# Optimization experiments

Measured on AMD Instinct MI355X. Metric: run time of the kernel, lower is better.

The kernel has to match this reference:

```python
import jax, jax.numpy as jnp
import numpy as np

N_OUT = 4096
N_IN = 4096
N_SPARSE = 1024  # int(0.25 * N_IN)
BATCH, SEQ = 4, 2048


def setup_inputs() -> dict:
    key = jax.random.key(0)
    k1, k2, k3 = jax.random.split(key, 3)
    x = jax.random.normal(k1, (BATCH, SEQ, N_IN), dtype=jnp.float32)
    sparse_values = jax.random.normal(k2, (N_OUT, N_SPARSE), dtype=jnp.float32)
    # static equivalent of the boolean sparse_mask: sorted unique column indices
    sparse_idx = jnp.sort(jax.random.permutation(k3, N_IN)[:N_SPARSE]).astype(jnp.int64)
    return {"x": x, "sparse_values": sparse_values, "sparse_idx": sparse_idx}


def reference(x, sparse_values, sparse_idx):
    # x[..., mask] @ sparse_values.T  ->  gather columns then GEMM
    x_g = jnp.take(x, sparse_idx, axis=-1)          # [B, S, n_sparse]
    return jnp.einsum('bsk,ok->bso', x_g, sparse_values)  # [B, S, n_out]
```

## Files before the change

### kernel.cpp

```cpp
#include <hip/hip_runtime.h>
#include <hip/hip_bf16.h>

#define NOUT  4096
#define KDIM  1024
#define MROWS 8192

typedef __attribute__((ext_vector_type(8))) short bf16x8;
typedef __attribute__((ext_vector_type(16))) float f32x16;

__device__ __forceinline__ unsigned short f2bf(float f) {
  union { float f; unsigned int u; } c; c.f = f;
  unsigned int lsb = (c.u >> 16) & 1u;
  c.u += 0x7fffu + lsb;
  return (unsigned short)(c.u >> 16);
}

__device__ __forceinline__ void gload_lds16(const void* g, void* l) {
  __builtin_amdgcn_global_load_lds(
      (const __attribute__((address_space(1))) void*)g,
      (__attribute__((address_space(3))) void*)l, 16, 0, 0);
}

#define FENCE() asm volatile("" ::: "memory")
#define BAR() do { FENCE(); __builtin_amdgcn_s_barrier(); FENCE(); } while (0)
#define VMW(n) asm volatile("s_waitcnt vmcnt(" #n ")" ::: "memory")

__global__ __launch_bounds__(512) void prep(const float* __restrict__ x,
                                            const void* __restrict__ idx_raw,
                                            const float* __restrict__ w,
                                            unsigned short* __restrict__ xg,
                                            unsigned short* __restrict__ wb) {
  const int b = blockIdx.x;
  const int t = threadIdx.x;

  if (b < 2048) {
    const long long* p64 = (const long long*)idx_raw;
    const bool is64 = ((unsigned long long)p64[0]) < 4096ull;
    const float* xb = x + (size_t)b * 4 * 4096;
    ushort4* dst = (ushort4*)(xg + (size_t)b * 4 * 1024);
#pragma unroll
    for (int i = 0; i < 2; ++i) {
      const int q = t + 512 * i;
      const int row = q >> 8;
      const int k = (q & 255) * 4;
      int ka0, ka1, ka2, ka3;
      if (is64) {
        longlong2 v0 = ((const longlong2*)p64)[(k >> 1) + 0];
        longlong2 v1 = ((const longlong2*)p64)[(k >> 1) + 1];
        ka0 = (int)v0.x; ka1 = (int)v0.y; ka2 = (int)v1.x; ka3 = (int)v1.y;
      } else {
        int4 v = ((const int4*)idx_raw)[k >> 2];
        ka0 = v.x; ka1 = v.y; ka2 = v.z; ka3 = v.w;
      }
      const float* rp = xb + row * 4096;
      ushort4 o;
      o.x = f2bf(rp[ka0]); o.y = f2bf(rp[ka1]);
      o.z = f2bf(rp[ka2]); o.w = f2bf(rp[ka3]);
      dst[q] = o;
    }
  } else {
    const int i0 = (b - 2048) * 2048 + t;
#pragma unroll
    for (int j = 0; j < 4; ++j) {
      float4 v = ((const float4*)w)[i0 + 512 * j];
      ushort4 o;
      o.x = f2bf(v.x); o.y = f2bf(v.y); o.z = f2bf(v.z); o.w = f2bf(v.w);
      ((ushort4*)wb)[i0 + 512 * j] = o;
    }
  }
}

__global__ __launch_bounds__(512, 2) void gemm256(const unsigned short* __restrict__ A,
                                                  const unsigned short* __restrict__ B,
                                                  float* __restrict__ C) {
  __shared__ __align__(16) unsigned short lds[65536];

  const int tid = threadIdx.x;
  const int lane = tid & 63;
  const int wid = tid >> 6;
  const int wm = wid >> 2, wn = wid & 3;
  const int l31 = lane & 31, lh = lane >> 5;

  const int bn0 = blockIdx.x * 256;
  const int bm0 = blockIdx.y * 256;

  const int pr = tid >> 3;
  const int cg = (tid & 7) ^ (pr & 7) ^ ((pr >> 3) & 3);
  const unsigned short* Ag = A + (size_t)(bm0 + pr) * KDIM + cg * 8;
  const unsigned short* Bg = B + (size_t)(bn0 + pr) * KDIM + cg * 8;
  const int tid8 = tid * 8;

  const int sw8 = (l31 & 7) ^ (l31 >> 3);
  const int cK0 = (lh ^ sw8) * 8;
  const int cK1 = cK0 ^ 16;
  const int cK2 = cK0 ^ 32;
  const int cK3 = cK0 ^ 48;
  const int aRow = wm * 8192 + l31 * 64;
  const int bRow = 32768 + wn * 4096 + l31 * 64;

  f32x16 acc[4][2] = {};
  bf16x8 a[2][4], bN0[4], bN1[4];

#define LOAD_A(D, MH) do {                                                        \
    const unsigned short* _p = lds + (D) * 16384 + aRow + (MH) * 4096;            \
    a[0][0] = *(const bf16x8*)(_p + cK0);        a[0][1] = *(const bf16x8*)(_p + cK1);         \
    a[0][2] = *(const bf16x8*)(_p + cK2);        a[0][3] = *(const bf16x8*)(_p + cK3);         \
    a[1][0] = *(const bf16x8*)(_p + 2048 + cK0); a[1][1] = *(const bf16x8*)(_p + 2048 + cK1);  \
    a[1][2] = *(const bf16x8*)(_p + 2048 + cK2); a[1][3] = *(const bf16x8*)(_p + 2048 + cK3);  \
  } while (0)

#define LOAD_B(D, NF, R) do {                                                     \
    const unsigned short* _p = lds + (D) * 16384 + bRow + (NF) * 2048;            \
    R[0] = *(const bf16x8*)(_p + cK0); R[1] = *(const bf16x8*)(_p + cK1);         \
    R[2] = *(const bf16x8*)(_p + cK2); R[3] = *(const bf16x8*)(_p + cK3);         \
  } while (0)

#define STAGE_A(D, T, H) do {                                                     \
    gload_lds16(Ag + (size_t)((H) * 128) * KDIM + (T) * 64,                       \
                lds + (D) * 16384 + (H) * 8192 + tid8);                           \
    gload_lds16(Ag + (size_t)((H) * 128 + 64) * KDIM + (T) * 64,                  \
                lds + (D) * 16384 + (H) * 8192 + 4096 + tid8);                    \
  } while (0)

#define STAGE_B(D, T, H) do {                                                     \
    gload_lds16(Bg + (size_t)((H) * 128) * KDIM + (T) * 64,                       \
                lds + 32768 + (D) * 16384 + (H) * 8192 + tid8);                   \
    gload_lds16(Bg + (size_t)((H) * 128 + 64) * KDIM + (T) * 64,                  \
                lds + 32768 + (D) * 16384 + (H) * 8192 + 4096 + tid8);            \
  } while (0)

#define MFMA_Q(MH, NH, R) do {                                                    \
    __builtin_amdgcn_s_setprio(1);                                                \
    _Pragma("unroll") for (int kb = 0; kb < 4; ++kb) {                            \
      _Pragma("unroll") for (int mf = 0; mf < 2; ++mf) {                          \
        acc[(MH)*2+mf][NH] = __builtin_amdgcn_mfma_f32_32x32x16_bf16(             \
            a[mf][kb], R[kb], acc[(MH)*2+mf][NH], 0, 0, 0);                       \
      }                                                                           \
    }                                                                             \
    __builtin_amdgcn_s_setprio(0);                                                \
  } while (0)

  STAGE_B(0, 0, 0); STAGE_B(0, 0, 1);
  STAGE_A(0, 0, 0); STAGE_A(0, 0, 1);
  STAGE_B(1, 1, 0); STAGE_B(1, 1, 1);
  VMW(4);
  BAR();

  for (int i = 0; i < 8; ++i) {
    const int tA1 = 2 * i + 1;
    const int tN0 = (2 * i + 2) & 15;
    const int tN1 = (2 * i + 3) & 15;

    LOAD_A(0, 0); LOAD_B(0, 0, bN0); STAGE_A(1, tA1, 0);
    BAR(); MFMA_Q(0, 0, bN0); BAR();
    LOAD_B(0, 1, bN1); STAGE_A(1, tA1, 1);
    BAR(); MFMA_Q(0, 1, bN1); BAR();
    LOAD_A(0, 1); STAGE_B(0, tN0, 0);
    BAR(); MFMA_Q(1, 0, bN0); BAR();
    STAGE_B(0, tN0, 1);
    BAR(); MFMA_Q(1, 1, bN1); VMW(4); BAR();
    LOAD_A(1, 0); LOAD_B(1, 0, bN0); STAGE_A(0, tN0, 0);
    BAR(); MFMA_Q(0, 0, bN0); BAR();
    LOAD_B(1, 1, bN1); STAGE_A(0, tN0, 1);
    BAR(); MFMA_Q(0, 1, bN1); BAR();
    LOAD_A(1, 1); STAGE_B(1, tN1, 0);
    BAR(); MFMA_Q(1, 0, bN0); BAR();
    STAGE_B(1, tN1, 1);
    BAR(); MFMA_Q(1, 1, bN1); VMW(4); BAR();
  }

  VMW(0);
  float* base = C + (size_t)(bm0 + wm * 128) * NOUT + bn0 + wn * 64;
#pragma unroll
  for (int mf = 0; mf < 4; ++mf)
#pragma unroll
    for (int nf = 0; nf < 2; ++nf) {
      f32x16 v = acc[mf][nf];
#pragma unroll
      for (int r = 0; r < 16; ++r) {
        const int rowi = mf * 32 + (r & 3) + 8 * (r >> 2) + 4 * lh;
        base[(size_t)rowi * NOUT + nf * 32 + l31] = v[r];
      }
    }

#undef LOAD_A
#undef LOAD_B
#undef STAGE_A
#undef STAGE_B
#undef MFMA_Q
}

extern "C" void kernel_launch(void* const* d_in, const int* in_sizes, int n_in,
                              void* d_out, int out_size, void* d_ws, size_t ws_size,
                              hipStream_t stream) {
  const float* x   = (const float*)d_in[0];
  const float* sv  = (const float*)d_in[1];
  const void*  idx = d_in[2];
  float* out = (float*)d_out;

  unsigned short* xg = (unsigned short*)d_ws;
  unsigned short* wb = xg + (size_t)MROWS * KDIM;

  prep<<<2560, 512, 0, stream>>>(x, idx, sv, xg, wb);

  dim3 grid(NOUT / 256, MROWS / 256);
  gemm256<<<grid, 512, 0, stream>>>(xg, wb, out);
}
```

Measured before the change: 114.6 us.

## Fuse column gather and bf16 conversion of x into the GEMM A-tile staging

Removes the separate gather/convert pass over x. The GEMM now loads the indexed fp32 columns directly from global memory into registers, converts them with packed bf16 conversion, and writes them to LDS, software-pipelined one stage ahead. Indices are cached in LDS, and the block-to-tile mapping is remapped so neighbouring blocks share x rows. This saves the intermediate write/read of the gathered activations, but each GEMM block reads x via scattered 4-byte loads that are re-fetched by every N-tile (16 blocks per M tile). It also raises register pressure and vmcnt bookkeeping.

```diff
diff --git a/kernel.cpp b/kernel.cpp
--- a/kernel.cpp
+++ b/kernel.cpp
@@ -15,6 +15,12 @@
   return (unsigned short)(c.u >> 16);
 }
 
+__device__ __forceinline__ unsigned cvtpk(float lo, float hi) {
+  unsigned r;
+  asm("v_cvt_pk_bf16_f32 %0, %1, %2" : "=v"(r) : "v"(lo), "v"(hi));
+  return r;
+}
+
 __device__ __forceinline__ void gload_lds16(const void* g, void* l) {
   __builtin_amdgcn_global_load_lds(
       (const __attribute__((address_space(1))) void*)g,
@@ -24,56 +30,27 @@
 #define FENCE() asm volatile("" ::: "memory")
 #define BAR() do { FENCE(); __builtin_amdgcn_s_barrier(); FENCE(); } while (0)
 #define VMW(n) asm volatile("s_waitcnt vmcnt(" #n ")" ::: "memory")
-
-__global__ __launch_bounds__(512) void prep(const float* __restrict__ x,
-                                            const void* __restrict__ idx_raw,
-                                            const float* __restrict__ w,
-                                            unsigned short* __restrict__ xg,
-                                            unsigned short* __restrict__ wb) {
-  const int b = blockIdx.x;
-  const int t = threadIdx.x;
-
-  if (b < 2048) {
-    const long long* p64 = (const long long*)idx_raw;
-    const bool is64 = ((unsigned long long)p64[0]) < 4096ull;
-    const float* xb = x + (size_t)b * 4 * 4096;
-    ushort4* dst = (ushort4*)(xg + (size_t)b * 4 * 1024);
-#pragma unroll
-    for (int i = 0; i < 2; ++i) {
-      const int q = t + 512 * i;
-      const int row = q >> 8;
-      const int k = (q & 255) * 4;
-      int ka0, ka1, ka2, ka3;
-      if (is64) {
-        longlong2 v0 = ((const longlong2*)p64)[(k >> 1) + 0];
-        longlong2 v1 = ((const longlong2*)p64)[(k >> 1) + 1];
-        ka0 = (int)v0.x; ka1 = (int)v0.y; ka2 = (int)v1.x; ka3 = (int)v1.y;
-      } else {
-        int4 v = ((const int4*)idx_raw)[k >> 2];
-        ka0 = v.x; ka1 = v.y; ka2 = v.z; ka3 = v.w;
-      }
-      const float* rp = xb + row * 4096;
-      ushort4 o;
-      o.x = f2bf(rp[ka0]); o.y = f2bf(rp[ka1]);
-      o.z = f2bf(rp[ka2]); o.w = f2bf(rp[ka3]);
-      dst[q] = o;
-    }
-  } else {
-    const int i0 = (b - 2048) * 2048 + t;
-#pragma unroll
-    for (int j = 0; j < 4; ++j) {
-      float4 v = ((const float4*)w)[i0 + 512 * j];
-      ushort4 o;
-      o.x = f2bf(v.x); o.y = f2bf(v.y); o.z = f2bf(v.z); o.w = f2bf(v.w);
-      ((ushort4*)wb)[i0 + 512 * j] = o;
-    }
+#define LGKM0() asm volatile("s_waitcnt lgkmcnt(0)" ::: "memory")
+
+__global__ __launch_bounds__(512) void prep_w(const float* __restrict__ w,
+                                              unsigned short* __restrict__ wb) {
+  const int i0 = blockIdx.x * 1024 + threadIdx.x;
+#pragma unroll
+  for (int j = 0; j < 2; ++j) {
+    const int i = i0 + 512 * j;
+    float4 v = ((const float4*)w)[i];
+    ushort4 o;
+    o.x = f2bf(v.x); o.y = f2bf(v.y); o.z = f2bf(v.z); o.w = f2bf(v.w);
+    ((ushort4*)wb)[i] = o;
   }
 }
 
-__global__ __launch_bounds__(512, 2) void gemm256(const unsigned short* __restrict__ A,
-                                                  const unsigned short* __restrict__ B,
-                                                  float* __restrict__ C) {
-  __shared__ __align__(16) unsigned short lds[65536];
+__global__ __launch_bounds__(512, 2) void gemmf(const float* __restrict__ x,
+                                                const void* __restrict__ idx_raw,
+                                                const unsigned short* __restrict__ Bw,
+                                                float* __restrict__ C) {
+  __shared__ __align__(16) unsigned short lds[65536 + 2048];
+  int* sidxB = (int*)(lds + 65536);
 
   const int tid = threadIdx.x;
   const int lane = tid & 63;
@@ -81,14 +58,29 @@
   const int wm = wid >> 2, wn = wid & 3;
   const int l31 = lane & 31, lh = lane >> 5;
 
-  const int bn0 = blockIdx.x * 256;
-  const int bm0 = blockIdx.y * 256;
+  const int bid = blockIdx.x;
+  const int bm0 = ((bid & 7) * 4 + (bid >> 7)) * 256;
+  const int bn0 = ((bid >> 3) & 15) * 256;
 
   const int pr = tid >> 3;
   const int cg = (tid & 7) ^ (pr & 7) ^ ((pr >> 3) & 3);
-  const unsigned short* Ag = A + (size_t)(bm0 + pr) * KDIM + cg * 8;
-  const unsigned short* Bg = B + (size_t)(bn0 + pr) * KDIM + cg * 8;
+  const unsigned short* Bg = Bw + (size_t)(bn0 + pr) * KDIM + cg * 8;
   const int tid8 = tid * 8;
+  const char* xb = (const char*)(x + (size_t)bm0 * 4096);
+
+  {
+    const long long* p64 = (const long long*)idx_raw;
+    const int* p32 = (const int*)idx_raw;
+    const bool is64 = ((unsigned long long)p64[0]) < 4096ull;
+    if (is64) {
+      sidxB[tid] = ((int)p64[tid]) << 2;
+      sidxB[tid + 512] = ((int)p64[tid + 512]) << 2;
+    } else {
+      sidxB[tid] = p32[tid] << 2;
+      sidxB[tid + 512] = p32[tid + 512] << 2;
+    }
+  }
+  LGKM0(); BAR();
 
   const int sw8 = (l31 & 7) ^ (l31 >> 3);
   const int cK0 = (lh ^ sw8) * 8;
@@ -100,6 +92,42 @@
 
   f32x16 acc[4][2] = {};
   bf16x8 a[2][4], bN0[4], bN1[4];
+  float gE0[16], gE1[16], gO0[16], gO1[16];
+
+#define LDX(boff) (*(const float*)(xb + (boff)))
+
+#define GA_ISSUE(T, H, S) do {                                                    \
+    const int _kb = (T) * 64 + cg * 8;                                            \
+    const int4 _o1 = *(const int4*)&sidxB[_kb];                                   \
+    const int4 _o2 = *(const int4*)&sidxB[_kb + 4];                               \
+    const int _r1 = ((H) * 128 + pr) << 14;                                       \
+    const int _r2 = _r1 + (64 << 14);                                             \
+    S[0] = LDX(_r1 + _o1.x);  S[1] = LDX(_r1 + _o1.y);                            \
+    S[2] = LDX(_r1 + _o1.z);  S[3] = LDX(_r1 + _o1.w);                            \
+    S[4] = LDX(_r1 + _o2.x);  S[5] = LDX(_r1 + _o2.y);                            \
+    S[6] = LDX(_r1 + _o2.z);  S[7] = LDX(_r1 + _o2.w);                            \
+    S[8] = LDX(_r2 + _o1.x);  S[9] = LDX(_r2 + _o1.y);                            \
+    S[10] = LDX(_r2 + _o1.z); S[11] = LDX(_r2 + _o1.w);                           \
+    S[12] = LDX(_r2 + _o2.x); S[13] = LDX(_r2 + _o2.y);                           \
+    S[14] = LDX(_r2 + _o2.z); S[15] = LDX(_r2 + _o2.w);                           \
+  } while (0)
+
+#define GA_WRITE(D, H, S) do {                                                    \
+    uint4 _u1, _u2;                                                               \
+    _u1.x = cvtpk(S[0], S[1]);   _u1.y = cvtpk(S[2], S[3]);                       \
+    _u1.z = cvtpk(S[4], S[5]);   _u1.w = cvtpk(S[6], S[7]);                       \
+    _u2.x = cvtpk(S[8], S[9]);   _u2.y = cvtpk(S[10], S[11]);                     \
+    _u2.z = cvtpk(S[12], S[13]); _u2.w = cvtpk(S[14], S[15]);                     \
+    *(uint4*)(lds + (D) * 16384 + (H) * 8192 + tid8) = _u1;                       \
+    *(uint4*)(lds + (D) * 16384 + (H) * 8192 + 4096 + tid8) = _u2;                \
+  } while (0)
+
+#define STAGE_B(D, T, H) do {                                                     \
+    gload_lds16(Bg + (size_t)((H) * 128) * KDIM + (T) * 64,                       \
+                lds + 32768 + (D) * 16384 + (H) * 8192 + tid8);                   \
+    gload_lds16(Bg + (size_t)((H) * 128 + 64) * KDIM + (T) * 64,                  \
+                lds + 32768 + (D) * 16384 + (H) * 8192 + 4096 + tid8);            \
+  } while (0)
 
 #define LOAD_A(D, MH) do {                                                        \
     const unsigned short* _p = lds + (D) * 16384 + aRow + (MH) * 4096;            \
@@ -113,20 +141,6 @@
     const unsigned short* _p = lds + (D) * 16384 + bRow + (NF) * 2048;            \
     R[0] = *(const bf16x8*)(_p + cK0); R[1] = *(const bf16x8*)(_p + cK1);         \
     R[2] = *(const bf16x8*)(_p + cK2); R[3] = *(const bf16x8*)(_p + cK3);         \
-  } while (0)
-
-#define STAGE_A(D, T, H) do {                                                     \
-    gload_lds16(Ag + (size_t)((H) * 128) * KDIM + (T) * 64,                       \
-                lds + (D) * 16384 + (H) * 8192 + tid8);                           \
-    gload_lds16(Ag + (size_t)((H) * 128 + 64) * KDIM + (T) * 64,                  \
-                lds + (D) * 16384 + (H) * 8192 + 4096 + tid8);                    \
-  } while (0)
-
-#define STAGE_B(D, T, H) do {                                                     \
-    gload_lds16(Bg + (size_t)((H) * 128) * KDIM + (T) * 64,                       \
-                lds + 32768 + (D) * 16384 + (H) * 8192 + tid8);                   \
-    gload_lds16(Bg + (size_t)((H) * 128 + 64) * KDIM + (T) * 64,                  \
-                lds + 32768 + (D) * 16384 + (H) * 8192 + 4096 + tid8);            \
   } while (0)
 
 #define MFMA_Q(MH, NH, R) do {                                                    \
@@ -140,33 +154,35 @@
     __builtin_amdgcn_s_setprio(0);                                                \
   } while (0)
 
+  GA_ISSUE(0, 0, gE0); GA_ISSUE(0, 1, gE1);
   STAGE_B(0, 0, 0); STAGE_B(0, 0, 1);
-  STAGE_A(0, 0, 0); STAGE_A(0, 0, 1);
-  STAGE_B(1, 1, 0); STAGE_B(1, 1, 1);
-  VMW(4);
-  BAR();
+  GA_WRITE(0, 0, gE0);
+  GA_WRITE(0, 1, gE1);
+  VMW(0);
+  GA_ISSUE(1, 0, gO0); STAGE_B(1, 1, 0);
+  GA_ISSUE(1, 1, gO1); STAGE_B(1, 1, 1);
+  LGKM0(); BAR();
 
   for (int i = 0; i < 8; ++i) {
-    const int tA1 = 2 * i + 1;
     const int tN0 = (2 * i + 2) & 15;
     const int tN1 = (2 * i + 3) & 15;
 
-    LOAD_A(0, 0); LOAD_B(0, 0, bN0); STAGE_A(1, tA1, 0);
+    LOAD_A(0, 0); LOAD_B(0, 0, bN0); GA_WRITE(1, 0, gO0); LGKM0();
     BAR(); MFMA_Q(0, 0, bN0); BAR();
-    LOAD_B(0, 1, bN1); STAGE_A(1, tA1, 1);
+    LOAD_B(0, 1, bN1); GA_WRITE(1, 1, gO1); LGKM0();
     BAR(); MFMA_Q(0, 1, bN1); BAR();
-    LOAD_A(0, 1); STAGE_B(0, tN0, 0);
+    LOAD_A(0, 1); GA_ISSUE(tN0, 0, gE0); STAGE_B(0, tN0, 0);
     BAR(); MFMA_Q(1, 0, bN0); BAR();
-    STAGE_B(0, tN0, 1);
-    BAR(); MFMA_Q(1, 1, bN1); VMW(4); BAR();
-    LOAD_A(1, 0); LOAD_B(1, 0, bN0); STAGE_A(0, tN0, 0);
+    GA_ISSUE(tN0, 1, gE1); STAGE_B(0, tN0, 1);
+    BAR(); MFMA_Q(1, 1, bN1); VMW(36); BAR();
+    LOAD_A(1, 0); LOAD_B(1, 0, bN0); GA_WRITE(0, 0, gE0); LGKM0();
     BAR(); MFMA_Q(0, 0, bN0); BAR();
-    LOAD_B(1, 1, bN1); STAGE_A(0, tN0, 1);
+    LOAD_B(1, 1, bN1); GA_WRITE(0, 1, gE1); LGKM0();
     BAR(); MFMA_Q(0, 1, bN1); BAR();
-    LOAD_A(1, 1); STAGE_B(1, tN1, 0);
+    LOAD_A(1, 1); GA_ISSUE(tN1, 0, gO0); STAGE_B(1, tN1, 0);
     BAR(); MFMA_Q(1, 0, bN0); BAR();
-    STAGE_B(1, tN1, 1);
-    BAR(); MFMA_Q(1, 1, bN1); VMW(4); BAR();
+    GA_ISSUE(tN1, 1, gO1); STAGE_B(1, tN1, 1);
+    BAR(); MFMA_Q(1, 1, bN1); VMW(36); BAR();
   }
 
   VMW(0);
@@ -183,10 +199,12 @@
       }
     }
 
+#undef LDX
+#undef GA_ISSUE
+#undef GA_WRITE
+#undef STAGE_B
 #undef LOAD_A
 #undef LOAD_B
-#undef STAGE_A
-#undef STAGE_B
 #undef MFMA_Q
 }
 
@@ -198,11 +216,8 @@
   const void*  idx = d_in[2];
   float* out = (float*)d_out;
 
-  unsigned short* xg = (unsigned short*)d_ws;
-  unsigned short* wb = xg + (size_t)MROWS * KDIM;
-
-  prep<<<2560, 512, 0, stream>>>(x, idx, sv, xg, wb);
-
-  dim3 grid(NOUT / 256, MROWS / 256);
-  gemm256<<<grid, 512, 0, stream>>>(xg, wb, out);
-}
+  unsigned short* wb = (unsigned short*)d_ws;
+
+  prep_w<<<1024, 512, 0, stream>>>(sv, wb);
+  gemmf<<<512, 512, 0, stream>>>(x, idx, wb, out);
+}
```

After: 365.9 us. +219.3%, slower.
